# Kernel optimization log

Measured on AMD Instinct MI355X. Metric: run time of the kernel, lower is better.

Reference implementation:

```python
import jax, jax.numpy as jnp
import numpy as np
import math

HEADS = 8


def setup_inputs() -> dict:
    key = jax.random.key(0)
    ks = jax.random.split(key, 6)
    B, N, H, R = 16, 1024, 512, 32
    s = lambda fan_in: 1.0 / math.sqrt(fan_in)
    return {
        "x": jax.random.normal(ks[0], (B, N, H), dtype=jnp.float32),
        "Wqkv": jax.random.normal(ks[1], (H, 3 * H), dtype=jnp.float32) * s(H),
        "bqkv": jnp.zeros((3 * H,), dtype=jnp.float32),
        "Wout": jax.random.normal(ks[2], (H, H), dtype=jnp.float32) * s(H),
        "bout": jnp.zeros((H,), dtype=jnp.float32),
        "u": jax.random.normal(ks[3], (N, R), dtype=jnp.float32) * s(R),
        "v": jax.random.normal(ks[4], (R, N), dtype=jnp.float32) * s(R),
    }


def reference(x, Wqkv, bqkv, Wout, bout, u, v):
    B, N, H = x.shape
    hd = H // HEADS
    # qkv projection -> [B, N, 3, heads, head_dim] -> split
    qkv = (x @ Wqkv + bqkv).reshape(B, N, 3, HEADS, hd)
    qkv = jnp.transpose(qkv, (2, 0, 3, 1, 4))  # [3, B, heads, N, hd]
    q, k, val = qkv[0], qkv[1], qkv[2]
    # feature map applied before the softmax branch too (as in source)
    q = jax.nn.elu(q) + 1.0
    k = jax.nn.elu(k) + 1.0
    # low-rank shared bias [N, N], broadcast over batch & heads
    bias = u @ v
    scores = jnp.einsum('bhnd,bhmd->bhnm', q, k) / math.sqrt(hd)
    attn = jax.nn.softmax(scores + bias[None, None, :, :], axis=-1)
    out = jnp.einsum('bhnm,bhme->bhne', attn, val)  # [B, heads, N, hd]
    out = jnp.transpose(out, (0, 2, 1, 3)).reshape(B, N, H)
    return out @ Wout + bout
```

## Files before the change

kernel.cpp:

```cpp
#include <hip/hip_runtime.h>
#include <hip/hip_bf16.h>

typedef unsigned short u16;
typedef __attribute__((ext_vector_type(8))) short short8;
typedef __attribute__((ext_vector_type(4))) float f32x4;
typedef __attribute__((ext_vector_type(16))) float f32x16;
typedef __attribute__((ext_vector_type(4))) int i32x4;
typedef __attribute__((ext_vector_type(2))) int i32x2;

#define MFMA16(a,b,c) __builtin_amdgcn_mfma_f32_16x16x32_bf16((a),(b),(c),0,0,0)
#define MFMA32(a,b,c) __builtin_amdgcn_mfma_f32_32x32x16_bf16((a),(b),(c),0,0,0)

__device__ __forceinline__ u16 f2bf(float f) {
  union { float f; unsigned int u; } x; x.f = f;
  unsigned int u = x.u;
  return (u16)((u + 0x7fffu + ((u >> 16) & 1u)) >> 16);
}

__device__ __forceinline__ unsigned cvtpk(float a, float b) {
  unsigned r;
  asm("v_cvt_pk_bf16_f32 %0, %1, %2" : "=v"(r) : "v"(a), "v"(b));
  return r;
}

__device__ __forceinline__ void gld16(const void* g, void* l) {
  __builtin_amdgcn_global_load_lds(
      (const __attribute__((address_space(1))) void*)g,
      (__attribute__((address_space(3))) void*)l, 16, 0, 0);
}

__global__ __launch_bounds__(256) void conv_bf16(
    const float* __restrict__ in, u16* __restrict__ out, int n8) {
  int i = blockIdx.x * 256 + threadIdx.x;
  if (i >= n8) return;
  f32x4 a = *(const f32x4*)(in + (size_t)i * 8);
  f32x4 b = *(const f32x4*)(in + (size_t)i * 8 + 4);
  union { short8 s; u16 u[8]; } r;
  #pragma unroll
  for (int j = 0; j < 4; ++j) { r.u[j] = f2bf(a[j]); r.u[4 + j] = f2bf(b[j]); }
  *(short8*)&out[(size_t)i * 8] = r.s;
}

__global__ __launch_bounds__(256) void transpose_bf16(
    const float* __restrict__ in, u16* __restrict__ out, int rows, int cols) {
  __shared__ float tile[32][33];
  int bc = blockIdx.x * 32, br = blockIdx.y * 32;
  int tx = threadIdx.x & 31, ty = threadIdx.x >> 5;
  #pragma unroll
  for (int i = ty; i < 32; i += 8)
    tile[i][tx] = in[(size_t)(br + i) * cols + bc + tx];
  __syncthreads();
  #pragma unroll
  for (int i = ty; i < 32; i += 8)
    out[(size_t)(bc + i) * rows + br + tx] = f2bf(tile[tx][i]);
}

__global__ __launch_bounds__(256) void vtrans(
    const u16* __restrict__ in, u16* __restrict__ out) {
  __shared__ u16 t[32][33];
  int bh = blockIdx.z;
  int n0 = blockIdx.y * 32, e0 = blockIdx.x * 32;
  int tx = threadIdx.x & 31, ty = threadIdx.x >> 5;
  size_t base = (size_t)bh << 16;
  #pragma unroll
  for (int i = ty; i < 32; i += 8)
    t[i][tx] = in[base + (size_t)(n0 + i) * 64 + e0 + tx];
  __syncthreads();
  #pragma unroll
  for (int i = ty; i < 32; i += 8)
    out[base + (size_t)(e0 + i) * 1024 + n0 + tx] = t[tx][i];
}

template<int MODE>
__global__ __launch_bounds__(256) void gemm128(
    const u16* __restrict__ A, const u16* __restrict__ Bt,
    const float* __restrict__ bias,
    u16* __restrict__ oq, u16* __restrict__ ok, u16* __restrict__ ov,
    float* __restrict__ fo) {
  const int K = 512;
  __shared__ __align__(16) u16 As[128 * 64];
  __shared__ __align__(16) u16 Bs[128 * 64];
  int tid = threadIdx.x;
  int w = tid >> 6, ln = tid & 63, lo = ln & 15, hi = ln >> 4;
  int wr = (w >> 1) * 64, wc = (w & 1) * 64;
  int bm = blockIdx.y * 128, bn = blockIdx.x * 128;

  f32x4 acc[4][4];
  #pragma unroll
  for (int m = 0; m < 4; ++m)
    #pragma unroll
    for (int n = 0; n < 4; ++n)
      acc[m][n] = (f32x4){0.f, 0.f, 0.f, 0.f};

  for (int k0 = 0; k0 < K; k0 += 64) {
    #pragma unroll
    for (int i = 0; i < 4; ++i) {
      int c = i * 256 + w * 64 + ln;
      int r = c >> 3, cc = c & 7;
      gld16(&A[(size_t)(bm + r) * K + k0 + ((cc ^ (r & 7)) << 3)], &As[c << 3]);
    }
    #pragma unroll
    for (int i = 0; i < 4; ++i) {
      int c = i * 256 + w * 64 + ln;
      int r = c >> 3, cc = c & 7;
      gld16(&Bt[(size_t)(bn + r) * K + k0 + ((cc ^ (r & 7)) << 3)], &Bs[c << 3]);
    }
    __syncthreads();
    #pragma unroll
    for (int ks = 0; ks < 2; ++ks) {
      short8 a[4], b[4];
      #pragma unroll
      for (int m = 0; m < 4; ++m) {
        int row = wr + m * 16 + lo;
        a[m] = *(const short8*)&As[row * 64 + (((ks * 4 + hi) ^ (lo & 7)) << 3)];
      }
      #pragma unroll
      for (int n = 0; n < 4; ++n) {
        int row = wc + n * 16 + lo;
        b[n] = *(const short8*)&Bs[row * 64 + (((ks * 4 + hi) ^ (lo & 7)) << 3)];
      }
      #pragma unroll
      for (int m = 0; m < 4; ++m)
        #pragma unroll
        for (int n = 0; n < 4; ++n)
          acc[m][n] = MFMA16(a[m], b[n], acc[m][n]);
    }
    __syncthreads();
  }
  #pragma unroll
  for (int m = 0; m < 4; ++m)
    #pragma unroll
    for (int n = 0; n < 4; ++n)
      #pragma unroll
      for (int r = 0; r < 4; ++r) {
        int row = bm + wr + m * 16 + hi * 4 + r;
        int col = bn + wc + n * 16 + lo;
        float v = acc[m][n][r] + bias[col];
        if (MODE == 0) {
          int type = col >> 9, hd = (col >> 6) & 7, e = col & 63;
          if (type < 2) { v = (v > 0.f) ? (v + 1.f) : __expf(v); if (type == 0) v *= 0.125f; }
          u16* dst = (type == 0) ? oq : ((type == 1) ? ok : ov);
          dst[(size_t)(((row >> 10) << 3) + hd) * 65536 + (size_t)(row & 1023) * 64 + e] = f2bf(v);
        } else {
          fo[(size_t)row * 512 + col] = v;
        }
      }
}

__global__ __launch_bounds__(256) void attn32(
    const u16* __restrict__ qh, const u16* __restrict__ kh,
    const u16* __restrict__ vt, const u16* __restrict__ ub,
    const u16* __restrict__ vtb, u16* __restrict__ ob) {
  __shared__ __align__(16) u16 Ks[64 * 64];
  __shared__ __align__(16) u16 Vs[64 * 64];
  __shared__ __align__(16) u16 Tb[64 * 32];
  int tid = threadIdx.x;
  int w = tid >> 6, ln = tid & 63;
  int m32 = ln & 31, h = ln >> 5;
  int bh = blockIdx.y;
  int q0 = blockIdx.x * 128 + w * 32;
  size_t bhb = (size_t)bh << 16;

  short8 qf[4], uf[2];
  #pragma unroll
  for (int ks = 0; ks < 4; ++ks)
    qf[ks] = *(const short8*)&qh[bhb + (size_t)(q0 + m32) * 64 + ks * 16 + h * 8];
  #pragma unroll
  for (int k2 = 0; k2 < 2; ++k2)
    uf[k2] = *(const short8*)&ub[(size_t)(q0 + m32) * 32 + k2 * 16 + h * 8];

  f32x16 o0 = {0.f,0.f,0.f,0.f,0.f,0.f,0.f,0.f,0.f,0.f,0.f,0.f,0.f,0.f,0.f,0.f};
  f32x16 o1 = o0;
  float mrun = -3e38f, lrun = 0.f;

  for (int kv = 0; kv < 1024; kv += 64) {
    #pragma unroll
    for (int i = 0; i < 2; ++i) {
      int c = i * 256 + w * 64 + ln;
      int r = c >> 3, cc = c & 7;
      gld16(&kh[bhb + (size_t)(kv + r) * 64 + ((cc ^ (r & 7)) << 3)], &Ks[c << 3]);
    }
    #pragma unroll
    for (int i = 0; i < 2; ++i) {
      int c = i * 256 + w * 64 + ln;
      int r = c >> 3, cc = c & 7;
      gld16(&vt[bhb + (size_t)r * 1024 + kv + ((cc ^ (r & 7)) << 3)], &Vs[c << 3]);
    }
    {
      int c = w * 64 + ln;
      int r = c >> 2, cc = c & 3;
      gld16(&vtb[(size_t)(kv + r) * 32 + ((cc ^ (r & 3)) << 3)], &Tb[c << 3]);
    }
    __syncthreads();

    f32x16 s0 = {0.f,0.f,0.f,0.f,0.f,0.f,0.f,0.f,0.f,0.f,0.f,0.f,0.f,0.f,0.f,0.f};
    f32x16 s1 = s0;
    #pragma unroll
    for (int k2 = 0; k2 < 2; ++k2) {
      int r0 = m32, r1 = 32 + m32;
      short8 t0 = *(const short8*)&Tb[r0 * 32 + (((k2 * 2 + h) ^ (r0 & 3)) << 3)];
      short8 t1 = *(const short8*)&Tb[r1 * 32 + (((k2 * 2 + h) ^ (r1 & 3)) << 3)];
      s0 = MFMA32(t0, uf[k2], s0);
      s1 = MFMA32(t1, uf[k2], s1);
    }
    #pragma unroll
    for (int ks = 0; ks < 4; ++ks) {
      int r0 = m32, r1 = 32 + m32;
      short8 k0f = *(const short8*)&Ks[r0 * 64 + (((ks * 2 + h) ^ (r0 & 7)) << 3)];
      short8 k1f = *(const short8*)&Ks[r1 * 64 + (((ks * 2 + h) ^ (r1 & 7)) << 3)];
      s0 = MFMA32(k0f, qf[ks], s0);
      s1 = MFMA32(k1f, qf[ks], s1);
    }

    float pm = fmaxf(s0[0], s1[0]);
    #pragma unroll
    for (int i = 1; i < 16; ++i) pm = fmaxf(pm, fmaxf(s0[i], s1[i]));
    pm = fmaxf(pm, __shfl_xor(pm, 32));
    if (__ballot(pm > mrun)) {
      float nm = fmaxf(mrun, pm);
      float al = __expf(mrun - nm);
      #pragma unroll
      for (int i = 0; i < 16; ++i) { o0[i] *= al; o1[i] *= al; }
      lrun *= al;
      mrun = nm;
    }
    float ls = 0.f;
    #pragma unroll
    for (int i = 0; i < 16; ++i) { float p = __expf(s0[i] - mrun); s0[i] = p; ls += p; }
    #pragma unroll
    for (int i = 0; i < 16; ++i) { float p = __expf(s1[i] - mrun); s1[i] = p; ls += p; }
    lrun += ls;

    unsigned pk0[4][2], pk1[4][2];
    #pragma unroll
    for (int r8 = 0; r8 < 4; ++r8) {
      pk0[r8][0] = cvtpk(s0[r8 * 4 + 0], s0[r8 * 4 + 1]);
      pk0[r8][1] = cvtpk(s0[r8 * 4 + 2], s0[r8 * 4 + 3]);
      pk1[r8][0] = cvtpk(s1[r8 * 4 + 0], s1[r8 * 4 + 1]);
      pk1[r8][1] = cvtpk(s1[r8 * 4 + 2], s1[r8 * 4 + 3]);
    }
    #pragma unroll
    for (int kvt = 0; kvt < 2; ++kvt) {
      #pragma unroll
      for (int msl = 0; msl < 2; ++msl) {
        unsigned a0 = kvt ? pk1[2 * msl][0] : pk0[2 * msl][0];
        unsigned b0 = kvt ? pk1[2 * msl + 1][0] : pk0[2 * msl + 1][0];
        unsigned a1 = kvt ? pk1[2 * msl][1] : pk0[2 * msl][1];
        unsigned b1 = kvt ? pk1[2 * msl + 1][1] : pk0[2 * msl + 1][1];
        asm("v_permlane32_swap_b32 %0, %1" : "+v"(a0), "+v"(b0));
        asm("v_permlane32_swap_b32 %0, %1" : "+v"(a1), "+v"(b1));
        union { i32x4 i; short8 s; } pu;
        pu.i = (i32x4){(int)a0, (int)a1, (int)b0, (int)b1};
        int ms = kvt * 2 + msl;
        int r0 = m32, r1 = 32 + m32;
        short8 v0 = *(const short8*)&Vs[r0 * 64 + (((ms * 2 + h) ^ (r0 & 7)) << 3)];
        short8 v1 = *(const short8*)&Vs[r1 * 64 + (((ms * 2 + h) ^ (r1 & 7)) << 3)];
        o0 = MFMA32(v0, pu.s, o0);
        o1 = MFMA32(v1, pu.s, o1);
      }
    }
    __syncthreads();
  }

  float lt = lrun + __shfl_xor(lrun, 32);
  float li = 1.f / lt;
  int b = bh >> 3, hd = bh & 7;
  size_t orow = ((size_t)(b * 1024 + q0 + m32)) * 512 + hd * 64;
  #pragma unroll
  for (int et = 0; et < 2; ++et) {
    #pragma unroll
    for (int r8 = 0; r8 < 4; ++r8) {
      float v0 = (et ? o1[r8 * 4 + 0] : o0[r8 * 4 + 0]) * li;
      float v1 = (et ? o1[r8 * 4 + 1] : o0[r8 * 4 + 1]) * li;
      float v2 = (et ? o1[r8 * 4 + 2] : o0[r8 * 4 + 2]) * li;
      float v3 = (et ? o1[r8 * 4 + 3] : o0[r8 * 4 + 3]) * li;
      i32x2 d = {(int)cvtpk(v0, v1), (int)cvtpk(v2, v3)};
      *(i32x2*)&ob[orow + et * 32 + 8 * r8 + 4 * h] = d;
    }
  }
}

extern "C" void kernel_launch(void* const* d_in, const int* in_sizes, int n_in,
                              void* d_out, int out_size, void* d_ws, size_t ws_size,
                              hipStream_t stream) {
  const float* x    = (const float*)d_in[0];
  const float* Wqkv = (const float*)d_in[1];
  const float* bqkv = (const float*)d_in[2];
  const float* Wout = (const float*)d_in[3];
  const float* bout = (const float*)d_in[4];
  const float* u    = (const float*)d_in[5];
  const float* vlr  = (const float*)d_in[6];
  float* out = (float*)d_out;

  char* ws = (char*)d_ws;
  u16* qh    = (u16*)(ws);
  u16* kh    = (u16*)(ws + 16777216);
  u16* xb    = (u16*)(ws + 33554432);
  u16* vTg   = (u16*)(ws + 33554432);
  u16* vtmp  = (u16*)(ws + 50331648);
  u16* ob    = (u16*)(ws + 50331648);
  u16* Wqkvt = (u16*)(ws + 67108864);
  u16* Woutt = (u16*)(ws + 68681728);
  u16* ub    = (u16*)(ws + 69206016);
  u16* vTb   = (u16*)(ws + 69271552);

  conv_bf16<<<4096, 256, 0, stream>>>(x, xb, 1048576);
  conv_bf16<<<16, 256, 0, stream>>>(u, ub, 4096);
  transpose_bf16<<<dim3(48, 16), 256, 0, stream>>>(Wqkv, Wqkvt, 512, 1536);
  transpose_bf16<<<dim3(16, 16), 256, 0, stream>>>(Wout, Woutt, 512, 512);
  transpose_bf16<<<dim3(32, 1), 256, 0, stream>>>(vlr, vTb, 32, 1024);
  gemm128<0><<<dim3(12, 128), 256, 0, stream>>>(xb, Wqkvt, bqkv, qh, kh, vtmp, nullptr);
  vtrans<<<dim3(2, 32, 128), 256, 0, stream>>>(vtmp, vTg);
  attn32<<<dim3(8, 128), 256, 0, stream>>>(qh, kh, vTg, ub, vTb, ob);
  gemm128<1><<<dim3(4, 128), 256, 0, stream>>>(ob, Woutt, bout, nullptr, nullptr, nullptr, out);
}
```

Measured before the change: 249.8 us.

## Double-buffer attention tiles, use exp2 softmax, fuse prep kernels, XCD-aware block mapping

Merges five small conversion and transpose launches into one prep kernel. Remaps block indices in the GEMM and attention kernels so neighbouring tiles land on the same XCD, for better L2 reuse. Double-buffers the K, V and bias tiles so the next tile's loads overlap the current tile's compute, and raises wave priority around the MFMAs. Folds log2(e) into the q scale and the u factor so the softmax can use the native v_exp_f32, and only rescales the running output when the max grows by more than a threshold. The lazy rescale trusts fp32 headroom and adds numeric risk, and the doubled LDS may lower occupancy.

```diff
diff --git a/kernel.cpp b/kernel.cpp
--- a/kernel.cpp
+++ b/kernel.cpp
@@ -23,29 +23,45 @@
   return r;
 }
 
+__device__ __forceinline__ float exp2v(float x) {
+  float r;
+  asm("v_exp_f32 %0, %1" : "=v"(r) : "v"(x));
+  return r;
+}
+
 __device__ __forceinline__ void gld16(const void* g, void* l) {
   __builtin_amdgcn_global_load_lds(
       (const __attribute__((address_space(1))) void*)g,
       (__attribute__((address_space(3))) void*)l, 16, 0, 0);
 }
 
-__global__ __launch_bounds__(256) void conv_bf16(
-    const float* __restrict__ in, u16* __restrict__ out, int n8) {
-  int i = blockIdx.x * 256 + threadIdx.x;
-  if (i >= n8) return;
-  f32x4 a = *(const f32x4*)(in + (size_t)i * 8);
-  f32x4 b = *(const f32x4*)(in + (size_t)i * 8 + 4);
-  union { short8 s; u16 u[8]; } r;
-  #pragma unroll
-  for (int j = 0; j < 4; ++j) { r.u[j] = f2bf(a[j]); r.u[4 + j] = f2bf(b[j]); }
-  *(short8*)&out[(size_t)i * 8] = r.s;
-}
-
-__global__ __launch_bounds__(256) void transpose_bf16(
-    const float* __restrict__ in, u16* __restrict__ out, int rows, int cols) {
+__global__ __launch_bounds__(256) void prep(
+    const float* __restrict__ x, u16* __restrict__ xb,
+    const float* __restrict__ u, u16* __restrict__ ub,
+    const float* __restrict__ Wqkv, u16* __restrict__ Wqkvt,
+    const float* __restrict__ Wout, u16* __restrict__ Woutt,
+    const float* __restrict__ vlr, u16* __restrict__ vTb) {
   __shared__ float tile[32][33];
-  int bc = blockIdx.x * 32, br = blockIdx.y * 32;
-  int tx = threadIdx.x & 31, ty = threadIdx.x >> 5;
+  int bid = blockIdx.x, tid = threadIdx.x;
+  if (bid < 4112) {
+    const float* in; u16* out; size_t i; float sc;
+    if (bid < 4096) { in = x; out = xb; i = (size_t)bid * 256 + tid; sc = 1.f; }
+    else { in = u; out = ub; i = (size_t)(bid - 4096) * 256 + tid; sc = 1.44269504f; }
+    f32x4 a = *(const f32x4*)(in + i * 8);
+    f32x4 b = *(const f32x4*)(in + i * 8 + 4);
+    union { short8 s; u16 us[8]; } r;
+    #pragma unroll
+    for (int j = 0; j < 4; ++j) { r.us[j] = f2bf(a[j] * sc); r.us[4 + j] = f2bf(b[j] * sc); }
+    *(short8*)&out[i * 8] = r.s;
+    return;
+  }
+  int tb = bid - 4112;
+  const float* in; u16* out; int rows, cols, bx, by;
+  if (tb < 768)       { in = Wqkv; out = Wqkvt; rows = 512; cols = 1536; bx = tb % 48; by = tb / 48; }
+  else if (tb < 1024) { int q = tb - 768; in = Wout; out = Woutt; rows = 512; cols = 512; bx = q % 16; by = q / 16; }
+  else                { in = vlr; out = vTb; rows = 32; cols = 1024; bx = tb - 1024; by = 0; }
+  int bc = bx * 32, br = by * 32;
+  int tx = tid & 31, ty = tid >> 5;
   #pragma unroll
   for (int i = ty; i < 32; i += 8)
     tile[i][tx] = in[(size_t)(br + i) * cols + bc + tx];
@@ -83,7 +99,12 @@
   int tid = threadIdx.x;
   int w = tid >> 6, ln = tid & 63, lo = ln & 15, hi = ln >> 4;
   int wr = (w >> 1) * 64, wc = (w & 1) * 64;
-  int bm = blockIdx.y * 128, bn = blockIdx.x * 128;
+  int lin = blockIdx.y * gridDim.x + blockIdx.x;
+  int xcd = lin & 7, idx = lin >> 3;
+  int perx = gridDim.x, rows_per = gridDim.y >> 3;
+  int by = xcd * rows_per + idx / perx;
+  int bx = idx % perx;
+  int bm = by * 128, bn = bx * 128;
 
   f32x4 acc[4][4];
   #pragma unroll
@@ -138,7 +159,10 @@
         float v = acc[m][n][r] + bias[col];
         if (MODE == 0) {
           int type = col >> 9, hd = (col >> 6) & 7, e = col & 63;
-          if (type < 2) { v = (v > 0.f) ? (v + 1.f) : __expf(v); if (type == 0) v *= 0.125f; }
+          if (type < 2) {
+            v = (v > 0.f) ? (v + 1.f) : __expf(v);
+            if (type == 0) v *= 0.18033688f;
+          }
           u16* dst = (type == 0) ? oq : ((type == 1) ? ok : ov);
           dst[(size_t)(((row >> 10) << 3) + hd) * 65536 + (size_t)(row & 1023) * 64 + e] = f2bf(v);
         } else {
@@ -147,18 +171,20 @@
       }
 }
 
-__global__ __launch_bounds__(256) void attn32(
+__global__ __launch_bounds__(256, 4) void attn32(
     const u16* __restrict__ qh, const u16* __restrict__ kh,
     const u16* __restrict__ vt, const u16* __restrict__ ub,
     const u16* __restrict__ vtb, u16* __restrict__ ob) {
-  __shared__ __align__(16) u16 Ks[64 * 64];
-  __shared__ __align__(16) u16 Vs[64 * 64];
-  __shared__ __align__(16) u16 Tb[64 * 32];
+  __shared__ __align__(16) u16 Ks[2][64 * 64];
+  __shared__ __align__(16) u16 Vs[2][64 * 64];
+  __shared__ __align__(16) u16 Tb[2][64 * 32];
   int tid = threadIdx.x;
   int w = tid >> 6, ln = tid & 63;
   int m32 = ln & 31, h = ln >> 5;
-  int bh = blockIdx.y;
-  int q0 = blockIdx.x * 128 + w * 32;
+  int lin = blockIdx.y * 8 + blockIdx.x;
+  int xcd = lin & 7, idx = lin >> 3;
+  int bh = xcd * 16 + (idx >> 3);
+  int q0 = (idx & 7) * 128 + w * 32;
   size_t bhb = (size_t)bh << 16;
 
   short8 qf[4], uf[2];
@@ -168,57 +194,66 @@
   #pragma unroll
   for (int k2 = 0; k2 < 2; ++k2)
     uf[k2] = *(const short8*)&ub[(size_t)(q0 + m32) * 32 + k2 * 16 + h * 8];
+
+  auto STAGE = [&](int buf, int kv) {
+    #pragma unroll
+    for (int i = 0; i < 2; ++i) {
+      int c = i * 256 + w * 64 + ln;
+      int r = c >> 3, cc = c & 7;
+      gld16(&kh[bhb + (size_t)(kv + r) * 64 + ((cc ^ (r & 7)) << 3)], &Ks[buf][c << 3]);
+    }
+    #pragma unroll
+    for (int i = 0; i < 2; ++i) {
+      int c = i * 256 + w * 64 + ln;
+      int r = c >> 3, cc = c & 7;
+      gld16(&vt[bhb + (size_t)r * 1024 + kv + ((cc ^ (r & 7)) << 3)], &Vs[buf][c << 3]);
+    }
+    {
+      int c = w * 64 + ln;
+      int r = c >> 2, cc = c & 3;
+      gld16(&vtb[(size_t)(kv + r) * 32 + ((cc ^ (r & 3)) << 3)], &Tb[buf][c << 3]);
+    }
+  };
 
   f32x16 o0 = {0.f,0.f,0.f,0.f,0.f,0.f,0.f,0.f,0.f,0.f,0.f,0.f,0.f,0.f,0.f,0.f};
   f32x16 o1 = o0;
   float mrun = -3e38f, lrun = 0.f;
 
-  for (int kv = 0; kv < 1024; kv += 64) {
-    #pragma unroll
-    for (int i = 0; i < 2; ++i) {
-      int c = i * 256 + w * 64 + ln;
-      int r = c >> 3, cc = c & 7;
-      gld16(&kh[bhb + (size_t)(kv + r) * 64 + ((cc ^ (r & 7)) << 3)], &Ks[c << 3]);
-    }
-    #pragma unroll
-    for (int i = 0; i < 2; ++i) {
-      int c = i * 256 + w * 64 + ln;
-      int r = c >> 3, cc = c & 7;
-      gld16(&vt[bhb + (size_t)r * 1024 + kv + ((cc ^ (r & 7)) << 3)], &Vs[c << 3]);
-    }
-    {
-      int c = w * 64 + ln;
-      int r = c >> 2, cc = c & 3;
-      gld16(&vtb[(size_t)(kv + r) * 32 + ((cc ^ (r & 3)) << 3)], &Tb[c << 3]);
-    }
-    __syncthreads();
+  int cur = 0;
+  STAGE(0, 0);
+  __syncthreads();
+
+  for (int t = 0; t < 16; ++t) {
+    if (t < 15) STAGE(cur ^ 1, (t + 1) * 64);
 
     f32x16 s0 = {0.f,0.f,0.f,0.f,0.f,0.f,0.f,0.f,0.f,0.f,0.f,0.f,0.f,0.f,0.f,0.f};
     f32x16 s1 = s0;
+    __builtin_amdgcn_s_setprio(1);
     #pragma unroll
     for (int k2 = 0; k2 < 2; ++k2) {
       int r0 = m32, r1 = 32 + m32;
-      short8 t0 = *(const short8*)&Tb[r0 * 32 + (((k2 * 2 + h) ^ (r0 & 3)) << 3)];
-      short8 t1 = *(const short8*)&Tb[r1 * 32 + (((k2 * 2 + h) ^ (r1 & 3)) << 3)];
+      short8 t0 = *(const short8*)&Tb[cur][r0 * 32 + (((k2 * 2 + h) ^ (r0 & 3)) << 3)];
+      short8 t1 = *(const short8*)&Tb[cur][r1 * 32 + (((k2 * 2 + h) ^ (r1 & 3)) << 3)];
       s0 = MFMA32(t0, uf[k2], s0);
       s1 = MFMA32(t1, uf[k2], s1);
     }
     #pragma unroll
     for (int ks = 0; ks < 4; ++ks) {
       int r0 = m32, r1 = 32 + m32;
-      short8 k0f = *(const short8*)&Ks[r0 * 64 + (((ks * 2 + h) ^ (r0 & 7)) << 3)];
-      short8 k1f = *(const short8*)&Ks[r1 * 64 + (((ks * 2 + h) ^ (r1 & 7)) << 3)];
+      short8 k0f = *(const short8*)&Ks[cur][r0 * 64 + (((ks * 2 + h) ^ (r0 & 7)) << 3)];
+      short8 k1f = *(const short8*)&Ks[cur][r1 * 64 + (((ks * 2 + h) ^ (r1 & 7)) << 3)];
       s0 = MFMA32(k0f, qf[ks], s0);
       s1 = MFMA32(k1f, qf[ks], s1);
     }
+    __builtin_amdgcn_s_setprio(0);
 
     float pm = fmaxf(s0[0], s1[0]);
     #pragma unroll
     for (int i = 1; i < 16; ++i) pm = fmaxf(pm, fmaxf(s0[i], s1[i]));
     pm = fmaxf(pm, __shfl_xor(pm, 32));
-    if (__ballot(pm > mrun)) {
+    if (!__all(pm - mrun <= 11.5f)) {
       float nm = fmaxf(mrun, pm);
-      float al = __expf(mrun - nm);
+      float al = exp2v(mrun - nm);
       #pragma unroll
       for (int i = 0; i < 16; ++i) { o0[i] *= al; o1[i] *= al; }
       lrun *= al;
@@ -226,9 +261,9 @@
     }
     float ls = 0.f;
     #pragma unroll
-    for (int i = 0; i < 16; ++i) { float p = __expf(s0[i] - mrun); s0[i] = p; ls += p; }
-    #pragma unroll
-    for (int i = 0; i < 16; ++i) { float p = __expf(s1[i] - mrun); s1[i] = p; ls += p; }
+    for (int i = 0; i < 16; ++i) { float p = exp2v(s0[i] - mrun); s0[i] = p; ls += p; }
+    #pragma unroll
+    for (int i = 0; i < 16; ++i) { float p = exp2v(s1[i] - mrun); s1[i] = p; ls += p; }
     lrun += ls;
 
     unsigned pk0[4][2], pk1[4][2];
@@ -253,13 +288,16 @@
         pu.i = (i32x4){(int)a0, (int)a1, (int)b0, (int)b1};
         int ms = kvt * 2 + msl;
         int r0 = m32, r1 = 32 + m32;
-        short8 v0 = *(const short8*)&Vs[r0 * 64 + (((ms * 2 + h) ^ (r0 & 7)) << 3)];
-        short8 v1 = *(const short8*)&Vs[r1 * 64 + (((ms * 2 + h) ^ (r1 & 7)) << 3)];
+        short8 v0 = *(const short8*)&Vs[cur][r0 * 64 + (((ms * 2 + h) ^ (r0 & 7)) << 3)];
+        short8 v1 = *(const short8*)&Vs[cur][r1 * 64 + (((ms * 2 + h) ^ (r1 & 7)) << 3)];
+        __builtin_amdgcn_s_setprio(1);
         o0 = MFMA32(v0, pu.s, o0);
         o1 = MFMA32(v1, pu.s, o1);
+        __builtin_amdgcn_s_setprio(0);
       }
     }
     __syncthreads();
+    cur ^= 1;
   }
 
   float lt = lrun + __shfl_xor(lrun, 32);
@@ -304,11 +342,7 @@
   u16* ub    = (u16*)(ws + 69206016);
   u16* vTb   = (u16*)(ws + 69271552);
 
-  conv_bf16<<<4096, 256, 0, stream>>>(x, xb, 1048576);
-  conv_bf16<<<16, 256, 0, stream>>>(u, ub, 4096);
-  transpose_bf16<<<dim3(48, 16), 256, 0, stream>>>(Wqkv, Wqkvt, 512, 1536);
-  transpose_bf16<<<dim3(16, 16), 256, 0, stream>>>(Wout, Woutt, 512, 512);
-  transpose_bf16<<<dim3(32, 1), 256, 0, stream>>>(vlr, vTb, 32, 1024);
+  prep<<<5168, 256, 0, stream>>>(x, xb, u, ub, Wqkv, Wqkvt, Wout, Woutt, vlr, vTb);
   gemm128<0><<<dim3(12, 128), 256, 0, stream>>>(xb, Wqkvt, bqkv, qh, kh, vtmp, nullptr);
   vtrans<<<dim3(2, 32, 128), 256, 0, stream>>>(vtmp, vTg);
   attn32<<<dim3(8, 128), 256, 0, stream>>>(qh, kh, vTg, ub, vTb, ob);
```

Result: faster. 220.5 us (-11.7%).
